# Kernel tuning notes

Measured on AMD Instinct MI355X. Metric: run time of the kernel, lower is better.

## Reference

```python
import jax, jax.numpy as jnp
import numpy as np

B, S, D_IN, D_OUT, H = 4, 2048, 1024, 1024, 16
D_HEAD = D_OUT // H


def setup_inputs() -> dict:
    key = jax.random.key(0)
    ks = jax.random.split(key, 6)
    sc = 0.02
    return {
        "x": jax.random.normal(ks[0], (B, S, D_IN), dtype=jnp.float32),
        "Wq": jax.random.normal(ks[1], (D_IN, D_OUT), dtype=jnp.float32) * sc,
        "Wk": jax.random.normal(ks[2], (D_IN, D_OUT), dtype=jnp.float32) * sc,
        "Wv": jax.random.normal(ks[3], (D_IN, D_OUT), dtype=jnp.float32) * sc,
        "Wo": jax.random.normal(ks[4], (D_OUT, D_OUT), dtype=jnp.float32) * sc,
        "bo": jnp.zeros((D_OUT,), dtype=jnp.float32),
    }


def reference(x, Wq, Wk, Wv, Wo, bo):
    n_batch, n_tok, _ = x.shape
    # QKV projections (no bias), reshape to [B, H, S, Dh]
    q = (x @ Wq).reshape(n_batch, n_tok, H, D_HEAD).transpose(0, 2, 1, 3)
    k = (x @ Wk).reshape(n_batch, n_tok, H, D_HEAD).transpose(0, 2, 1, 3)
    v = (x @ Wv).reshape(n_batch, n_tok, H, D_HEAD).transpose(0, 2, 1, 3)
    # scores [B, H, S, S], causal mask, scaled softmax
    scores = jnp.einsum('bhqd,bhkd->bhqk', q, k)
    causal = jnp.tril(jnp.ones((n_tok, n_tok), dtype=bool))
    scores = jnp.where(causal, scores, -jnp.inf)
    attn = jax.nn.softmax(scores / jnp.sqrt(jnp.float32(D_HEAD)), axis=-1)
    # dropout in eval mode -> identity
    ctx = jnp.einsum('bhqk,bhkd->bhqd', attn, v)
    ctx = ctx.transpose(0, 2, 1, 3).reshape(n_batch, n_tok, D_OUT)
    return ctx @ Wo + bo
```

## Files before the change

### kernel.cpp

```cpp
#include <hip/hip_runtime.h>


#define S_LEN 2048
#define DMODEL 1024
#define NB 4

typedef unsigned short u16;
typedef unsigned int u32;
typedef float f32x4 __attribute__((ext_vector_type(4)));
typedef float f32x16 __attribute__((ext_vector_type(16)));
typedef int i32x4 __attribute__((ext_vector_type(4)));
typedef short s16x8 __attribute__((ext_vector_type(8)));
typedef __bf16 bf16x8 __attribute__((ext_vector_type(8)));

__device__ __forceinline__ u16 f2bf(float f) {
  return __builtin_bit_cast(u16, (__bf16)f);
}

__device__ __forceinline__ f32x4 mfma16(s16x8 a, s16x8 b, f32x4 c) {
  return __builtin_amdgcn_mfma_f32_16x16x32_bf16(
      __builtin_bit_cast(bf16x8, a), __builtin_bit_cast(bf16x8, b), c, 0, 0, 0);
}

__device__ __forceinline__ f32x16 mfma32(s16x8 a, s16x8 b, f32x16 c) {
  return __builtin_amdgcn_mfma_f32_32x32x16_bf16(
      __builtin_bit_cast(bf16x8, a), __builtin_bit_cast(bf16x8, b), c, 0, 0, 0);
}

__device__ __forceinline__ int cvtpk(float a, float b) {
  int r;
  asm("v_cvt_pk_bf16_f32 %0, %1, %2" : "=v"(r) : "v"(a), "v"(b));
  return r;
}

__device__ __forceinline__ void gload_lds16(void* lds, const void* g) {
  __builtin_amdgcn_global_load_lds(
      (const __attribute__((address_space(1))) void*)g,
      (__attribute__((address_space(3))) void*)lds, 16, 0, 0);
}

__device__ __forceinline__ s16x8 lds_frag(const u16* lds, int row, int colb) {
  int addr = (row << 7) + (colb ^ ((row & 7) << 4));
  return *(const s16x8*)((const char*)lds + addr);
}

struct G8 {
  u16 As[3][256 * 64];
  u16 Bs[3][128 * 64];
};

template <int NT>
__device__ __forceinline__ void gemm8ph(const u16* __restrict__ A,
                                        const u16* __restrict__ Bt,
                                        int m0, int n0, G8& L,
                                        f32x4 (&acc)[4][4], int tid) {
  constexpr int K = NT * 64;
  const int lane = tid & 63;
  const int wr = (tid >> 6) >> 1, wc = (tid >> 6) & 1;

  auto SA = [&](int buf, int kt) {
    const u16* g = A + (size_t)m0 * K + kt * 64;
    #pragma unroll
    for (int it = 0; it < 4; ++it) {
      int o = (tid + it * 512) << 4;
      int r = o >> 7, c = o & 127;
      gload_lds16((char*)L.As[buf] + o,
                  (const char*)(g + (size_t)r * K) + (c ^ ((r & 7) << 4)));
    }
  };
  auto SB = [&](int buf, int kt) {
    const u16* g = Bt + (size_t)n0 * K + kt * 64;
    #pragma unroll
    for (int it = 0; it < 2; ++it) {
      int o = (tid + it * 512) << 4;
      int r = o >> 7, c = o & 127;
      gload_lds16((char*)L.Bs[buf] + o,
                  (const char*)(g + (size_t)r * K) + (c ^ ((r & 7) << 4)));
    }
  };

  SA(0, 0); SB(0, 0);
  SA(1, 1); SB(1, 1);
  asm volatile("s_waitcnt vmcnt(6)" ::: "memory");
  asm volatile("s_barrier" ::: "memory");

  int cb = 0;
  for (int t = 0; t < NT; ++t) {
    const u16* Ac = L.As[cb];
    const u16* Bc = L.Bs[cb];
    int nxt = cb + 2; if (nxt >= 3) nxt -= 3;
    bool pf = (t + 2 < NT);
    #pragma unroll
    for (int ph = 0; ph < 2; ++ph) {
      s16x8 a[4], b[4];
      #pragma unroll
      for (int f = 0; f < 4; ++f) {
        a[f] = lds_frag(Ac, wr * 64 + f * 16 + (lane & 15), ph * 64 + ((lane >> 4) << 4));
        b[f] = lds_frag(Bc, wc * 64 + f * 16 + (lane & 15), ph * 64 + ((lane >> 4) << 4));
      }
      if (pf) { if (ph == 0) SA(nxt, t + 2); else SB(nxt, t + 2); }
      asm volatile("s_barrier" ::: "memory");
      asm volatile("s_waitcnt lgkmcnt(0)" ::: "memory");
      __builtin_amdgcn_sched_barrier(0);
      __builtin_amdgcn_s_setprio(1);
      #pragma unroll
      for (int mf = 0; mf < 4; ++mf)
        #pragma unroll
        for (int nf = 0; nf < 4; ++nf)
          acc[mf][nf] = mfma16(a[mf], b[nf], acc[mf][nf]);
      __builtin_amdgcn_s_setprio(0);
    }
    if (pf) asm volatile("s_waitcnt vmcnt(6)" ::: "memory");
    else    asm volatile("s_waitcnt vmcnt(0)" ::: "memory");
    asm volatile("s_barrier" ::: "memory");
    cb = (cb + 1 == 3) ? 0 : cb + 1;
  }
}

__global__ __launch_bounds__(256) void castx_kernel(const float4* __restrict__ x,
                                                    ushort4* __restrict__ xb) {
  int i = blockIdx.x * 256 + threadIdx.x;
  float4 v = x[i];
  ushort4 o;
  o.x = f2bf(v.x); o.y = f2bf(v.y); o.z = f2bf(v.z); o.w = f2bf(v.w);
  xb[i] = o;
}

__global__ __launch_bounds__(256) void wtrans_kernel(
    const float* __restrict__ W0, const float* __restrict__ W1,
    const float* __restrict__ W2, const float* __restrict__ W3,
    u16* __restrict__ T0, u16* __restrict__ T1, u16* __restrict__ T2, u16* __restrict__ T3) {
  int z = blockIdx.z;
  const float* W = (z == 0) ? W0 : (z == 1) ? W1 : (z == 2) ? W2 : W3;
  u16* T = (z == 0) ? T0 : (z == 1) ? T1 : (z == 2) ? T2 : T3;
  __shared__ float t[32][33];
  int n0 = blockIdx.x << 5, k0 = blockIdx.y << 5;
  int tx = threadIdx.x & 31, ty = threadIdx.x >> 5;
  #pragma unroll
  for (int j = 0; j < 4; ++j)
    t[ty + (j << 3)][tx] = W[(size_t)(k0 + ty + (j << 3)) * DMODEL + n0 + tx];
  __syncthreads();
  #pragma unroll
  for (int j = 0; j < 4; ++j)
    T[(size_t)(n0 + ty + (j << 3)) * DMODEL + k0 + tx] = f2bf(t[tx][ty + (j << 3)]);
}

__global__ __launch_bounds__(512, 2) void qkv8_kernel(
    const u16* __restrict__ xb, const u16* __restrict__ WqkvT,
    u16* __restrict__ Qo, u16* __restrict__ Ko, u16* __restrict__ Vo) {
  __shared__ G8 L;
  int bid = blockIdx.x;
  int f = (bid & 7) * 96 + (bid >> 3);
  int m0 = (f / 24) << 8, n0 = (f % 24) << 7;
  int tid = threadIdx.x, lane = tid & 63;
  int wr = (tid >> 6) >> 1, wc = (tid >> 6) & 1;
  f32x4 acc[4][4] = {};
  gemm8ph<16>(xb, WqkvT, m0, n0, L, acc, tid);
  #pragma unroll
  for (int mf = 0; mf < 4; ++mf)
    #pragma unroll
    for (int nf = 0; nf < 4; ++nf)
      #pragma unroll
      for (int i = 0; i < 4; ++i) {
        int rm = m0 + wr * 64 + mf * 16 + ((lane >> 4) << 2) + i;
        int cn = n0 + wc * 64 + nf * 16 + (lane & 15);
        int bb = rm >> 11, s = rm & (S_LEN - 1);
        int z = cn >> 10, c1 = cn & 1023;
        int h = c1 >> 6, d = c1 & 63;
        u16* out = (z == 0) ? Qo : (z == 1) ? Ko : Vo;
        float v = acc[mf][nf][i] * ((z == 0) ? 0.18033688f : 1.0f);
        out[((size_t)((bb << 4) + h) << 17) + ((size_t)s << 6) + d] = f2bf(v);
      }
}

__global__ __launch_bounds__(256) void vtrans_kernel(const u16* __restrict__ V,
                                                     u16* __restrict__ Vt) {
  __shared__ u16 t[64][72];
  int s0 = blockIdx.x << 6;
  size_t bh = blockIdx.y;
  const u16* Vb = V + (bh << 17);
  u16* Vtb = Vt + (bh << 17);
  int tid = threadIdx.x;
  #pragma unroll
  for (int it = 0; it < 2; ++it) {
    int o = (tid + (it << 8)) << 3;
    int r = o >> 6, c = o & 63;
    const ushort4* p = (const ushort4*)(Vb + (((size_t)(s0 + r)) << 6) + c);
    ushort4 v0 = p[0], v1 = p[1];
    t[r][c + 0] = v0.x; t[r][c + 1] = v0.y; t[r][c + 2] = v0.z; t[r][c + 3] = v0.w;
    t[r][c + 4] = v1.x; t[r][c + 5] = v1.y; t[r][c + 6] = v1.z; t[r][c + 7] = v1.w;
  }
  __syncthreads();
  #pragma unroll
  for (int it = 0; it < 2; ++it) {
    int o = (tid + (it << 8)) << 3;
    int d = o >> 6, sl = o & 63;
    ushort4 a, b;
    a.x = t[sl + 0][d]; a.y = t[sl + 1][d]; a.z = t[sl + 2][d]; a.w = t[sl + 3][d];
    b.x = t[sl + 4][d]; b.y = t[sl + 5][d]; b.z = t[sl + 6][d]; b.w = t[sl + 7][d];
    ushort4* q = (ushort4*)(Vtb + ((size_t)d << 11) + s0 + sl);
    q[0] = a; q[1] = b;
  }
}

__global__ __launch_bounds__(256, 2) void attn_kernel(const u16* __restrict__ Q,
                                                      const u16* __restrict__ K,
                                                      const u16* __restrict__ Vt,
                                                      u16* __restrict__ ctx) {
  __shared__ u16 Ks[2][64 * 64];
  __shared__ u16 Vts[2][64 * 64];
  int bh = blockIdx.x, pid = blockIdx.y;
  int tid = threadIdx.x, lane = tid & 63, w = tid >> 6;
  int hi = lane >> 5, lq = lane & 31;
  const u16* Qb = Q + ((size_t)bh << 17);
  const u16* Kb = K + ((size_t)bh << 17);
  const u16* Vtb = Vt + ((size_t)bh << 17);
  int bb = bh >> 4, h = bh & 15;

  auto stage = [&](int buf, int k0) {
    #pragma unroll
    for (int it = 0; it < 2; ++it) {
      int o = (tid + (it << 8)) << 4;
      int r = o >> 7, c = o & 127;
      int csrc = c ^ ((r & 7) << 4);
      gload_lds16((char*)Ks[buf] + o, (const char*)(Kb + ((size_t)(k0 + r) << 6)) + csrc);
      gload_lds16((char*)Vts[buf] + o, (const char*)(Vtb + ((size_t)r << 11) + k0) + csrc);
    }
  };

  for (int ph = 0; ph < 2; ++ph) {
    int qblk = ph ? (15 - pid) : pid;
    int q0 = qblk << 7;
    int qw = q0 + (w << 5);
    int q = qw + lq;

    s16x8 qf[4];
    #pragma unroll
    for (int t = 0; t < 4; ++t)
      qf[t] = *(const s16x8*)(Qb + ((size_t)q << 6) + t * 16 + (hi << 3));

    f32x16 acc_o[2] = {};
    float l_acc = 0.0f;

    int ntiles = (q0 >> 6) + 2;
    int cur = 0;
    stage(0, 0);
    __syncthreads();
    for (int t = 0; t < ntiles; ++t) {
      int k0 = t << 6;
      if (t + 1 < ntiles) stage(cur ^ 1, (t + 1) << 6);
      const u16* Kc = Ks[cur];
      const u16* Vc = Vts[cur];

      #pragma unroll
      for (int kvb = 0; kvb < 2; ++kvb) {
        int kb0 = k0 + kvb * 32;
        if (kb0 <= qw + 31) {
          f32x16 sc = {};
          #pragma unroll
          for (int tt = 0; tt < 4; ++tt) {
            s16x8 kf = lds_frag(Kc, kvb * 32 + lq, tt * 32 + (hi << 4));
            sc = mfma32(kf, qf[tt], sc);
          }
          if (kb0 + 31 > qw) {
            #pragma unroll
            for (int r = 0; r < 16; ++r) {
              int kv = kb0 + (r & 3) + ((r >> 2) << 3) + (hi << 2);
              sc[r] = (kv <= q) ? sc[r] : -3.0e38f;
            }
          }
          #pragma unroll
          for (int r = 0; r < 16; ++r) sc[r] = __builtin_amdgcn_exp2f(sc[r]);
          #pragma unroll
          for (int r = 0; r < 16; ++r) l_acc += sc[r];

          #pragma unroll
          for (int tt = 0; tt < 2; ++tt) {
            int x0 = cvtpk(sc[8 * tt + 0], sc[8 * tt + 1]);
            int x1 = cvtpk(sc[8 * tt + 2], sc[8 * tt + 3]);
            int y0 = cvtpk(sc[8 * tt + 4], sc[8 * tt + 5]);
            int y1 = cvtpk(sc[8 * tt + 6], sc[8 * tt + 7]);
            asm volatile("v_permlane32_swap_b32 %0, %1" : "+v"(x0), "+v"(y0));
            asm volatile("v_permlane32_swap_b32 %0, %1" : "+v"(x1), "+v"(y1));
            i32x4 wi = {x0, x1, y0, y1};
            s16x8 W = __builtin_bit_cast(s16x8, wi);
            int tg = kvb * 2 + tt;
            __builtin_amdgcn_s_setprio(1);
            #pragma unroll
            for (int dblk = 0; dblk < 2; ++dblk) {
              s16x8 vf = lds_frag(Vc, dblk * 32 + lq, tg * 32 + (hi << 4));
              acc_o[dblk] = mfma32(vf, W, acc_o[dblk]);
            }
            __builtin_amdgcn_s_setprio(0);
          }
        }
      }
      __syncthreads();
      cur ^= 1;
    }

    l_acc += __shfl_xor(l_acc, 32);
    float linv = 1.0f / l_acc;
    #pragma unroll
    for (int dblk = 0; dblk < 2; ++dblk)
      #pragma unroll
      for (int rp = 0; rp < 8; ++rp) {
        int r = rp * 2;
        int pk = cvtpk(acc_o[dblk][r] * linv, acc_o[dblk][r + 1] * linv);
        int d = dblk * 32 + (r & 3) + ((r >> 2) << 3) + (hi << 2);
        *(u32*)(ctx + (((size_t)(bb << 11) + q) << 10) + (h << 6) + d) = (u32)pk;
      }
  }
}

__global__ __launch_bounds__(512, 2) void out8_kernel(const u16* __restrict__ ctx,
                                                      const u16* __restrict__ WoT,
                                                      const float* __restrict__ bo,
                                                      float* __restrict__ out) {
  __shared__ G8 L;
  int bid = blockIdx.x;
  int f = (bid & 7) * 32 + (bid >> 3);
  int m0 = (f >> 3) << 8, n0 = (f & 7) << 7;
  int tid = threadIdx.x, lane = tid & 63;
  int wr = (tid >> 6) >> 1, wc = (tid >> 6) & 1;
  f32x4 acc[4][4] = {};
  gemm8ph<16>(ctx, WoT, m0, n0, L, acc, tid);
  #pragma unroll
  for (int mf = 0; mf < 4; ++mf)
    #pragma unroll
    for (int nf = 0; nf < 4; ++nf)
      #pragma unroll
      for (int i = 0; i < 4; ++i) {
        int rm = m0 + wr * 64 + mf * 16 + ((lane >> 4) << 2) + i;
        int cn = n0 + wc * 64 + nf * 16 + (lane & 15);
        out[(size_t)rm * DMODEL + cn] = acc[mf][nf][i] + bo[cn];
      }
}

extern "C" void kernel_launch(void* const* d_in, const int* in_sizes, int n_in,
                              void* d_out, int out_size, void* d_ws, size_t ws_size,
                              hipStream_t stream) {
  const float* x  = (const float*)d_in[0];
  const float* Wq = (const float*)d_in[1];
  const float* Wk = (const float*)d_in[2];
  const float* Wv = (const float*)d_in[3];
  const float* Wo = (const float*)d_in[4];
  const float* bo = (const float*)d_in[5];
  float* out = (float*)d_out;

  char* ws = (char*)d_ws;
  const size_t SZ_T = (size_t)NB * S_LEN * DMODEL * 2;
  const size_t SZ_W = (size_t)DMODEL * DMODEL * 2;
  u16* xb  = (u16*)(ws);
  u16* WqT = (u16*)(ws + SZ_T);
  u16* WkT = (u16*)(ws + SZ_T + 1 * SZ_W);
  u16* WvT = (u16*)(ws + SZ_T + 2 * SZ_W);
  u16* WoT = (u16*)(ws + SZ_T + 3 * SZ_W);
  u16* Qb  = (u16*)(ws + 1 * SZ_T + 4 * SZ_W);
  u16* Kb  = (u16*)(ws + 2 * SZ_T + 4 * SZ_W);
  u16* Vb  = (u16*)(ws + 3 * SZ_T + 4 * SZ_W);
  u16* Vtb = (u16*)(ws + 4 * SZ_T + 4 * SZ_W);
  u16* ctx = xb;

  castx_kernel<<<dim3((NB * S_LEN * DMODEL / 4) / 256), dim3(256), 0, stream>>>(
      (const float4*)x, (ushort4*)xb);
  wtrans_kernel<<<dim3(32, 32, 4), dim3(256), 0, stream>>>(Wq, Wk, Wv, Wo,
                                                           WqT, WkT, WvT, WoT);
  qkv8_kernel<<<dim3(768), dim3(512), 0, stream>>>(xb, WqT, Qb, Kb, Vb);
  vtrans_kernel<<<dim3(32, 64), dim3(256), 0, stream>>>(Vb, Vtb);
  attn_kernel<<<dim3(64, 8), dim3(256), 0, stream>>>(Qb, Kb, Vtb, ctx);
  out8_kernel<<<dim3(256), dim3(512), 0, stream>>>(ctx, WoT, bo, out);
}
```

Baseline: 154.0 us.

## Use 256x256 QKV GEMM tiles and write V transposed directly

Replaces the 256x128 triple-buffered QKV GEMM with a 256x256 double-buffered tile (8 waves, 8x4 accumulators per wave), halving the grid to 384 blocks. The epilogue for the V third writes V already transposed into [B,H,D,S] via packed bf16 pairs, which removes the separate vtrans kernel and its extra global read and write. Risks include higher register and LDS use (128KB LDS per block, which may limit occupancy), strided 4-byte stores for Vt, and fewer blocks relative to CU count.

```diff
diff --git a/kernel.cpp b/kernel.cpp
--- a/kernel.cpp
+++ b/kernel.cpp
@@ -42,6 +42,75 @@
 __device__ __forceinline__ s16x8 lds_frag(const u16* lds, int row, int colb) {
   int addr = (row << 7) + (colb ^ ((row & 7) << 4));
   return *(const s16x8*)((const char*)lds + addr);
+}
+
+struct G256 {
+  u16 As[2][256 * 64];
+  u16 Bs[2][256 * 64];
+};
+
+template <int NT>
+__device__ __forceinline__ void gemm256(const u16* __restrict__ A,
+                                        const u16* __restrict__ Bt,
+                                        int m0, int n0, G256& L,
+                                        f32x4 (&acc)[8][4], int tid) {
+  constexpr int K = NT * 64;
+  const int lane = tid & 63;
+  const int wv = tid >> 6, wr = wv >> 2, wc = wv & 3;
+
+  auto ST = [&](int buf, int kt, int which) {
+    const u16* g = (which ? Bt + (size_t)n0 * K : A + (size_t)m0 * K) + kt * 64;
+    u16* dst = which ? L.Bs[buf] : L.As[buf];
+    #pragma unroll
+    for (int it = 0; it < 4; ++it) {
+      int o = (tid + it * 512) << 4;
+      int r = o >> 7, c = o & 127;
+      gload_lds16((char*)dst + o,
+                  (const char*)(g + (size_t)r * K) + (c ^ ((r & 7) << 4)));
+    }
+  };
+
+  ST(0, 0, 0); ST(0, 0, 1);
+  asm volatile("s_waitcnt vmcnt(0)" ::: "memory");
+  __syncthreads();
+
+  for (int kt = 0; kt < NT; ++kt) {
+    int p = kt & 1;
+    const u16* Ac = L.As[p];
+    const u16* Bc = L.Bs[p];
+    s16x8 bfr[4];
+    #pragma unroll
+    for (int ph = 0; ph < 4; ++ph) {
+      int ks = ph >> 1, mh = ph & 1;
+      if (mh == 0) {
+        #pragma unroll
+        for (int f = 0; f < 4; ++f)
+          bfr[f] = lds_frag(Bc, wc * 64 + f * 16 + (lane & 15),
+                            ks * 64 + ((lane >> 4) << 4));
+      }
+      s16x8 a[4];
+      #pragma unroll
+      for (int f = 0; f < 4; ++f)
+        a[f] = lds_frag(Ac, wr * 128 + mh * 64 + f * 16 + (lane & 15),
+                        ks * 64 + ((lane >> 4) << 4));
+      if (kt + 1 < NT) {
+        if (ph == 0) ST(p ^ 1, kt + 1, 0);
+        else if (ph == 1) ST(p ^ 1, kt + 1, 1);
+      }
+      __builtin_amdgcn_s_barrier();
+      asm volatile("s_waitcnt lgkmcnt(0)" ::: "memory");
+      __builtin_amdgcn_sched_barrier(0);
+      __builtin_amdgcn_s_setprio(1);
+      #pragma unroll
+      for (int mf = 0; mf < 4; ++mf)
+        #pragma unroll
+        for (int nf = 0; nf < 4; ++nf)
+          acc[mh * 4 + mf][nf] = mfma16(a[mf], bfr[nf], acc[mh * 4 + mf][nf]);
+      __builtin_amdgcn_s_setprio(0);
+      __builtin_amdgcn_s_barrier();
+    }
+    __syncthreads();
+  }
 }
 
 struct G8 {
@@ -145,61 +214,49 @@
     T[(size_t)(n0 + ty + (j << 3)) * DMODEL + k0 + tx] = f2bf(t[tx][ty + (j << 3)]);
 }
 
-__global__ __launch_bounds__(512, 2) void qkv8_kernel(
+__global__ __launch_bounds__(512, 2) void qkv256_kernel(
     const u16* __restrict__ xb, const u16* __restrict__ WqkvT,
-    u16* __restrict__ Qo, u16* __restrict__ Ko, u16* __restrict__ Vo) {
-  __shared__ G8 L;
+    u16* __restrict__ Qo, u16* __restrict__ Ko, u16* __restrict__ Vto) {
+  __shared__ G256 L;
   int bid = blockIdx.x;
-  int f = (bid & 7) * 96 + (bid >> 3);
-  int m0 = (f / 24) << 8, n0 = (f % 24) << 7;
+  int f = (bid & 7) * 48 + (bid >> 3);
+  int m0 = (f / 12) << 8, n0 = (f % 12) << 8;
   int tid = threadIdx.x, lane = tid & 63;
-  int wr = (tid >> 6) >> 1, wc = (tid >> 6) & 1;
-  f32x4 acc[4][4] = {};
-  gemm8ph<16>(xb, WqkvT, m0, n0, L, acc, tid);
-  #pragma unroll
-  for (int mf = 0; mf < 4; ++mf)
-    #pragma unroll
-    for (int nf = 0; nf < 4; ++nf)
-      #pragma unroll
-      for (int i = 0; i < 4; ++i) {
-        int rm = m0 + wr * 64 + mf * 16 + ((lane >> 4) << 2) + i;
+  int wv = tid >> 6, wr = wv >> 2, wc = wv & 3;
+  f32x4 acc[8][4] = {};
+  gemm256<16>(xb, WqkvT, m0, n0, L, acc, tid);
+
+  int z = n0 >> 10;
+  if (z == 2) {
+    #pragma unroll
+    for (int am = 0; am < 8; ++am)
+      #pragma unroll
+      for (int nf = 0; nf < 4; ++nf) {
+        int rm = m0 + wr * 128 + (am >> 2) * 64 + (am & 3) * 16 + ((lane >> 4) << 2);
         int cn = n0 + wc * 64 + nf * 16 + (lane & 15);
         int bb = rm >> 11, s = rm & (S_LEN - 1);
-        int z = cn >> 10, c1 = cn & 1023;
-        int h = c1 >> 6, d = c1 & 63;
-        u16* out = (z == 0) ? Qo : (z == 1) ? Ko : Vo;
-        float v = acc[mf][nf][i] * ((z == 0) ? 0.18033688f : 1.0f);
-        out[((size_t)((bb << 4) + h) << 17) + ((size_t)s << 6) + d] = f2bf(v);
-      }
-}
-
-__global__ __launch_bounds__(256) void vtrans_kernel(const u16* __restrict__ V,
-                                                     u16* __restrict__ Vt) {
-  __shared__ u16 t[64][72];
-  int s0 = blockIdx.x << 6;
-  size_t bh = blockIdx.y;
-  const u16* Vb = V + (bh << 17);
-  u16* Vtb = Vt + (bh << 17);
-  int tid = threadIdx.x;
-  #pragma unroll
-  for (int it = 0; it < 2; ++it) {
-    int o = (tid + (it << 8)) << 3;
-    int r = o >> 6, c = o & 63;
-    const ushort4* p = (const ushort4*)(Vb + (((size_t)(s0 + r)) << 6) + c);
-    ushort4 v0 = p[0], v1 = p[1];
-    t[r][c + 0] = v0.x; t[r][c + 1] = v0.y; t[r][c + 2] = v0.z; t[r][c + 3] = v0.w;
-    t[r][c + 4] = v1.x; t[r][c + 5] = v1.y; t[r][c + 6] = v1.z; t[r][c + 7] = v1.w;
-  }
-  __syncthreads();
-  #pragma unroll
-  for (int it = 0; it < 2; ++it) {
-    int o = (tid + (it << 8)) << 3;
-    int d = o >> 6, sl = o & 63;
-    ushort4 a, b;
-    a.x = t[sl + 0][d]; a.y = t[sl + 1][d]; a.z = t[sl + 2][d]; a.w = t[sl + 3][d];
-    b.x = t[sl + 4][d]; b.y = t[sl + 5][d]; b.z = t[sl + 6][d]; b.w = t[sl + 7][d];
-    ushort4* q = (ushort4*)(Vtb + ((size_t)d << 11) + s0 + sl);
-    q[0] = a; q[1] = b;
+        int c1 = cn & 1023, h = c1 >> 6, d = c1 & 63;
+        u32 p0 = (u32)cvtpk(acc[am][nf][0], acc[am][nf][1]);
+        u32 p1 = (u32)cvtpk(acc[am][nf][2], acc[am][nf][3]);
+        u32* dst = (u32*)(Vto + (((size_t)((bb << 4) + h)) << 17) + ((size_t)d << 11) + s);
+        dst[0] = p0; dst[1] = p1;
+      }
+  } else {
+    float scale = (z == 0) ? 0.18033688f : 1.0f;
+    u16* out = (z == 0) ? Qo : Ko;
+    #pragma unroll
+    for (int am = 0; am < 8; ++am)
+      #pragma unroll
+      for (int nf = 0; nf < 4; ++nf)
+        #pragma unroll
+        for (int i = 0; i < 4; ++i) {
+          int rm = m0 + wr * 128 + (am >> 2) * 64 + (am & 3) * 16 + ((lane >> 4) << 2) + i;
+          int cn = n0 + wc * 64 + nf * 16 + (lane & 15);
+          int bb = rm >> 11, s = rm & (S_LEN - 1);
+          int c1 = cn & 1023, h = c1 >> 6, d = c1 & 63;
+          out[((size_t)((bb << 4) + h) << 17) + ((size_t)s << 6) + d] =
+              f2bf(acc[am][nf][i] * scale);
+        }
   }
 }
 
@@ -358,16 +415,14 @@
   u16* WoT = (u16*)(ws + SZ_T + 3 * SZ_W);
   u16* Qb  = (u16*)(ws + 1 * SZ_T + 4 * SZ_W);
   u16* Kb  = (u16*)(ws + 2 * SZ_T + 4 * SZ_W);
-  u16* Vb  = (u16*)(ws + 3 * SZ_T + 4 * SZ_W);
-  u16* Vtb = (u16*)(ws + 4 * SZ_T + 4 * SZ_W);
+  u16* Vtb = (u16*)(ws + 3 * SZ_T + 4 * SZ_W);
   u16* ctx = xb;
 
   castx_kernel<<<dim3((NB * S_LEN * DMODEL / 4) / 256), dim3(256), 0, stream>>>(
       (const float4*)x, (ushort4*)xb);
   wtrans_kernel<<<dim3(32, 32, 4), dim3(256), 0, stream>>>(Wq, Wk, Wv, Wo,
                                                            WqT, WkT, WvT, WoT);
-  qkv8_kernel<<<dim3(768), dim3(512), 0, stream>>>(xb, WqT, Qb, Kb, Vb);
-  vtrans_kernel<<<dim3(32, 64), dim3(256), 0, stream>>>(Vb, Vtb);
+  qkv256_kernel<<<dim3(384), dim3(512), 0, stream>>>(xb, WqT, Qb, Kb, Vtb);
   attn_kernel<<<dim3(64, 8), dim3(256), 0, stream>>>(Qb, Kb, Vtb, ctx);
   out8_kernel<<<dim3(256), dim3(512), 0, stream>>>(ctx, WoT, bo, out);
 }
```

New measurement: 156.1 us. About the same (+1.4%).
